# Optimization experiments

Measured on AMD Instinct MI355X. Metric: run time of the kernel, lower is better.

Reference implementation:

```python
import jax, jax.numpy as jnp
import numpy as np

B, N = 16384, 4096
PERCENT_ON = 0.1
TEMPERATURE = 10.0  # training-mode temperature
K = int(round(N * PERCENT_ON))  # 410


def setup_inputs() -> dict:
    key = jax.random.key(0)
    k1, k2 = jax.random.split(key)
    x = jax.random.normal(k1, (B, N), dtype=jnp.float32)
    # Gumbel noise for sampling-without-replacement (Gumbel-top-k trick),
    # equivalent to torch.multinomial(softmax(x/T), k, replacement=False).
    gumbel = jax.random.gumbel(k2, (B, N), dtype=jnp.float32)
    return {"x": x, "gumbel": gumbel}


def reference(x, gumbel):
    # logits with temperature
    logits = x / TEMPERATURE
    # entropy of the categorical distribution per row, averaged (single stable pass)
    logp = jax.nn.log_softmax(logits, axis=-1)
    entropy = jnp.mean(-jnp.sum(jnp.exp(logp) * logp, axis=-1))
    # sample K winners without replacement via Gumbel-top-k
    _, idx = jax.lax.top_k(logits + gumbel, K)  # idx: [B, K]
    rows = jnp.arange(x.shape[0])[:, None]       # [B, 1]
    mask = jnp.zeros_like(x).at[rows, idx].set(1.0)
    out = x * mask  # relu=False path
    return out, entropy
```

## Files before the change

### kernel.cpp

```cpp
#include <hip/hip_runtime.h>
#include <math.h>

#define TPB 256
#define EPT 16
#define NN  4096
#define KSEL 410
#define CAP 1024

typedef float floatx4 __attribute__((ext_vector_type(4)));

template <bool USE_WS>
__global__ __launch_bounds__(TPB, 8)
void skw_main(const float* __restrict__ x, const float* __restrict__ g,
              float* __restrict__ out, float* __restrict__ rowH,
              float* __restrict__ entAcc, float invB)
{
    const int row  = blockIdx.x;
    const int t    = threadIdx.x;
    const int w    = t >> 6;
    const int lane = t & 63;
    const size_t rbase = (size_t)row * NN;

    float    xv[EPT];
    unsigned bp[EPT / 4];

    __shared__ float    s_lds[NN];
    __shared__ unsigned hist0[256][5];
    __shared__ unsigned wtot[4];
    __shared__ unsigned wtA[4], wtB[4];
    __shared__ float    fred[8];
    __shared__ unsigned sh_digit, sh_above, sh_cnt, sh_take, sh_eq;
    __shared__ float    sh_thr;

    float*   list = reinterpret_cast<float*>(&hist0[0][0]);
    floatx4* s4   = reinterpret_cast<floatx4*>(s_lds);

    const float4* xp = reinterpret_cast<const float4*>(x + rbase);
    const float4* gp = reinterpret_cast<const float4*>(g + rbase);
    floatx4*      op = reinterpret_cast<floatx4*>(out + rbase);

    float sZ = 0.f, sZL = 0.f;
#pragma unroll
    for (int q = 0; q < EPT / 4; ++q) {
        float4 xx = xp[(q << 8) + t];
        float4 gg = gp[(q << 8) + t];
        float xa[4] = {xx.x, xx.y, xx.z, xx.w};
        float ga[4] = {gg.x, gg.y, gg.z, gg.w};
        floatx4 so;
        unsigned pk = 0;
#pragma unroll
        for (int jj = 0; jj < 4; ++jj) {
            float xs = xa[jj];
            xv[4 * q + jj] = xs;
            float l = xs * 0.1f;
            float e = __expf(l);
            sZ  += e;
            sZL = __builtin_fmaf(e, l, sZL);
            float q10 = __builtin_fmaf(__builtin_fmaf(-10.0f, l, xs), 0.1f, l);
            float s = q10 + ga[jj];
            so[jj] = s;
            int b = (int)__builtin_fmaf(s, 16.0f, 64.0f);
            b = min(max(b, 0), 255);
            pk |= (unsigned)b << (8 * jj);
        }
        s4[(q << 8) + t] = so;
        bp[q] = pk;
    }

#pragma unroll
    for (int sft = 32; sft >= 1; sft >>= 1) { sZ += __shfl_xor(sZ, sft); sZL += __shfl_xor(sZL, sft); }
    if (lane == 0) { fred[w] = sZ; fred[4 + w] = sZL; }

    unsigned* h0 = &hist0[0][0];
#pragma unroll
    for (int i = 0; i < 5; ++i) h0[t + 256 * i] = 0;
    if (t == 0) sh_cnt = 0;
    __syncthreads();

    if (t == 0) {
        float Z = fred[0] + fred[1] + fred[2] + fred[3];
        float L = fred[4] + fred[5] + fred[6] + fred[7];
        float H = __logf(Z) - L / Z;
        if (USE_WS) rowH[row] = H;
        else atomicAdd(entAcc, H * invB);
    }

#pragma unroll
    for (int q = 0; q < EPT / 4; ++q) {
        unsigned pk = bp[q];
#pragma unroll
        for (int jj = 0; jj < 4; ++jj)
            atomicAdd(&hist0[(pk >> (8 * jj)) & 255u][lane & 3], 1u);
    }
    __syncthreads();

    unsigned v = hist0[t][0] + hist0[t][1] + hist0[t][2] + hist0[t][3];
#pragma unroll
    for (int sft = 1; sft < 64; sft <<= 1) {
        unsigned tmp = __shfl(v, lane + sft);
        v += (lane + sft < 64) ? tmp : 0u;
    }
    if (lane == 0) wtot[w] = v;
    unsigned vnext = __shfl(v, lane + 1);
    __syncthreads();
    unsigned Kr = KSEL;
    {
        unsigned hi = 0;
#pragma unroll
        for (int c = 0; c < 4; ++c) hi += (c > w) ? wtot[c] : 0u;
        unsigned cum     = v + hi;
        unsigned cumNext = ((lane < 63) ? vnext : 0u) + hi;
        if (cum >= Kr && cumNext < Kr) { sh_digit = (unsigned)t; sh_above = cumNext; }
    }
    __syncthreads();
    const unsigned Bstar = sh_digit;
    Kr -= sh_above;

#pragma unroll
    for (int q = 0; q < EPT / 4; ++q) {
        unsigned pk = bp[q];
#pragma unroll
        for (int jj = 0; jj < 4; ++jj) {
            if (((pk >> (8 * jj)) & 255u) == Bstar) {
                unsigned p = atomicAdd(&sh_cnt, 1u);
                if (p < CAP) list[p] = s_lds[(q << 10) + 4 * t + jj];
            }
        }
    }
    __syncthreads();

    const unsigned M = sh_cnt;
    for (unsigned i = t; i < M; i += TPB) {
        float ki = list[i];
        unsigned gt = 0, eqc = 0;
        for (unsigned j2 = 0; j2 < M; ++j2) {
            float kj = list[j2];
            gt  += (kj > ki)  ? 1u : 0u;
            eqc += (kj == ki) ? 1u : 0u;
        }
        if (gt < Kr && Kr <= gt + eqc) { sh_thr = ki; sh_take = Kr - gt; sh_eq = eqc; }
    }
    __syncthreads();
    const float    thr    = sh_thr;
    const unsigned KrTake = sh_take;
    const unsigned EqTot  = sh_eq;

    if (KrTake == EqTot) {
#pragma unroll
        for (int q = 0; q < EPT / 4; ++q) {
            floatx4 sq = s4[(q << 8) + t];
            floatx4 o4;
#pragma unroll
            for (int jj = 0; jj < 4; ++jj)
                o4[jj] = (sq[jj] >= thr) ? xv[4 * q + jj] : 0.0f;
            __builtin_nontemporal_store(o4, &op[(q << 8) + t]);
        }
    } else {
        unsigned eq[4];
#pragma unroll
        for (int q = 0; q < 4; ++q) {
            floatx4 sq = s4[(q << 8) + t];
            unsigned e = 0;
#pragma unroll
            for (int jj = 0; jj < 4; ++jj) e += (sq[jj] == thr) ? 1u : 0u;
            eq[q] = e;
        }
        unsigned wA = eq[0] | (eq[1] << 16);
        unsigned wB = eq[2] | (eq[3] << 16);
        unsigned sA = wA, sB = wB;
#pragma unroll
        for (int sft = 1; sft < 64; sft <<= 1) {
            unsigned ta = __shfl(sA, lane - sft);
            unsigned tb = __shfl(sB, lane - sft);
            if (lane >= sft) { sA += ta; sB += tb; }
        }
        if (lane == 63) { wtA[w] = sA; wtB[w] = sB; }
        __syncthreads();
        unsigned offA = 0, offB = 0, totA = 0, totB = 0;
#pragma unroll
        for (int c = 0; c < 4; ++c) {
            totA += wtA[c]; totB += wtB[c];
            if (c < w) { offA += wtA[c]; offB += wtB[c]; }
        }
        unsigned exA = offA + sA - wA;
        unsigned exB = offB + sB - wB;
        unsigned tot0 = totA & 0xFFFFu, tot1 = totA >> 16, tot2 = totB & 0xFFFFu;
        unsigned baseq[4] = {0u, tot0, tot0 + tot1, tot0 + tot1 + tot2};
        unsigned exq[4]   = {exA & 0xFFFFu, exA >> 16, exB & 0xFFFFu, exB >> 16};

#pragma unroll
        for (int q = 0; q < EPT / 4; ++q) {
            unsigned pos = baseq[q] + exq[q];
            floatx4 sq = s4[(q << 8) + t];
            floatx4 o4;
#pragma unroll
            for (int jj = 0; jj < 4; ++jj) {
                bool sel;
                if (sq[jj] > thr)        sel = true;
                else if (sq[jj] == thr)  { sel = (pos < KrTake); ++pos; }
                else                     sel = false;
                o4[jj] = sel ? xv[4 * q + jj] : 0.0f;
            }
            __builtin_nontemporal_store(o4, &op[(q << 8) + t]);
        }
    }
}

__global__ void skw_zero(float* p) { *p = 0.0f; }

__global__ void skw_reduce(const float* __restrict__ rowH, float* __restrict__ outp, int B)
{
    __shared__ float red[256];
    int t = threadIdx.x;
    float s = 0.f;
    for (int i = t; i < B; i += 256) s += rowH[i];
    red[t] = s; __syncthreads();
    for (int st = 128; st > 0; st >>= 1) { if (t < st) red[t] += red[t + st]; __syncthreads(); }
    if (t == 0) *outp = red[0] / (float)B;
}

extern "C" void kernel_launch(void* const* d_in, const int* in_sizes, int n_in,
                              void* d_out, int out_size, void* d_ws, size_t ws_size,
                              hipStream_t stream)
{
    const float* x = (const float*)d_in[0];
    const float* g = (const float*)d_in[1];
    float* out = (float*)d_out;
    const int BN = in_sizes[0];
    const int B  = BN / NN;
    float* entp = out + (size_t)BN;

    if (ws_size >= (size_t)B * sizeof(float)) {
        float* rowH = (float*)d_ws;
        skw_main<true><<<B, TPB, 0, stream>>>(x, g, out, rowH, nullptr, 0.f);
        skw_reduce<<<1, 256, 0, stream>>>(rowH, entp, B);
    } else {
        skw_zero<<<1, 1, 0, stream>>>(entp);
        skw_main<false><<<B, TPB, 0, stream>>>(x, g, out, nullptr, entp, 1.0f / (float)B);
    }
}
```

Measured before the change: 165.3 us.

## Stage x and gumbel rows into LDS via direct global-to-LDS loads

```diff
diff --git a/kernel.cpp b/kernel.cpp
--- a/kernel.cpp
+++ b/kernel.cpp
@@ -9,8 +9,15 @@
 
 typedef float floatx4 __attribute__((ext_vector_type(4)));
 
+__device__ __forceinline__ void dma16(const float* gsrc, float* lds) {
+    __builtin_amdgcn_global_load_lds(
+        (__attribute__((address_space(1))) void*)(void*)gsrc,
+        (__attribute__((address_space(3))) void*)(void*)lds,
+        16, 0, 0);
+}
+
 template <bool USE_WS>
-__global__ __launch_bounds__(TPB, 8)
+__global__ __launch_bounds__(TPB)
 void skw_main(const float* __restrict__ x, const float* __restrict__ g,
               float* __restrict__ out, float* __restrict__ rowH,
               float* __restrict__ entAcc, float invB)
@@ -21,10 +28,9 @@
     const int lane = t & 63;
     const size_t rbase = (size_t)row * NN;
 
-    float    xv[EPT];
     unsigned bp[EPT / 4];
 
-    __shared__ float    s_lds[NN];
+    __shared__ float    stage[2 * NN];
     __shared__ unsigned hist0[256][5];
     __shared__ unsigned wtot[4];
     __shared__ unsigned wtA[4], wtB[4];
@@ -33,48 +39,55 @@
     __shared__ float    sh_thr;
 
     float*   list = reinterpret_cast<float*>(&hist0[0][0]);
-    floatx4* s4   = reinterpret_cast<floatx4*>(s_lds);
-
-    const float4* xp = reinterpret_cast<const float4*>(x + rbase);
-    const float4* gp = reinterpret_cast<const float4*>(g + rbase);
-    floatx4*      op = reinterpret_cast<floatx4*>(out + rbase);
+    floatx4* sx4  = reinterpret_cast<floatx4*>(stage);
+    floatx4* ss4  = reinterpret_cast<floatx4*>(stage + NN);
+
+    const float* xr = x + rbase;
+    const float* gr = g + rbase;
+    floatx4*     op = reinterpret_cast<floatx4*>(out + rbase);
+
+#pragma unroll
+    for (int q = 0; q < 4; ++q) {
+        const int c = (q << 2) + w;
+        dma16(xr + (c << 8) + (lane << 2), &stage[c << 8]);
+        dma16(gr + (c << 8) + (lane << 2), &stage[NN + (c << 8)]);
+    }
+
+    unsigned* h0 = &hist0[0][0];
+#pragma unroll
+    for (int i = 0; i < 5; ++i) h0[t + 256 * i] = 0;
+    if (t == 0) sh_cnt = 0;
+
+    asm volatile("s_waitcnt vmcnt(0)" ::: "memory");
 
     float sZ = 0.f, sZL = 0.f;
 #pragma unroll
     for (int q = 0; q < EPT / 4; ++q) {
-        float4 xx = xp[(q << 8) + t];
-        float4 gg = gp[(q << 8) + t];
-        float xa[4] = {xx.x, xx.y, xx.z, xx.w};
-        float ga[4] = {gg.x, gg.y, gg.z, gg.w};
+        floatx4 xx = sx4[(q << 8) + t];
+        floatx4 gg = ss4[(q << 8) + t];
         floatx4 so;
         unsigned pk = 0;
 #pragma unroll
         for (int jj = 0; jj < 4; ++jj) {
-            float xs = xa[jj];
-            xv[4 * q + jj] = xs;
+            float xs = xx[jj];
             float l = xs * 0.1f;
             float e = __expf(l);
             sZ  += e;
             sZL = __builtin_fmaf(e, l, sZL);
             float q10 = __builtin_fmaf(__builtin_fmaf(-10.0f, l, xs), 0.1f, l);
-            float s = q10 + ga[jj];
+            float s = q10 + gg[jj];
             so[jj] = s;
             int b = (int)__builtin_fmaf(s, 16.0f, 64.0f);
             b = min(max(b, 0), 255);
             pk |= (unsigned)b << (8 * jj);
         }
-        s4[(q << 8) + t] = so;
+        ss4[(q << 8) + t] = so;
         bp[q] = pk;
     }
 
 #pragma unroll
     for (int sft = 32; sft >= 1; sft >>= 1) { sZ += __shfl_xor(sZ, sft); sZL += __shfl_xor(sZL, sft); }
     if (lane == 0) { fred[w] = sZ; fred[4 + w] = sZL; }
-
-    unsigned* h0 = &hist0[0][0];
-#pragma unroll
-    for (int i = 0; i < 5; ++i) h0[t + 256 * i] = 0;
-    if (t == 0) sh_cnt = 0;
     __syncthreads();
 
     if (t == 0) {
@@ -123,7 +136,7 @@
         for (int jj = 0; jj < 4; ++jj) {
             if (((pk >> (8 * jj)) & 255u) == Bstar) {
                 unsigned p = atomicAdd(&sh_cnt, 1u);
-                if (p < CAP) list[p] = s_lds[(q << 10) + 4 * t + jj];
+                if (p < CAP) list[p] = stage[NN + (q << 10) + 4 * t + jj];
             }
         }
     }
@@ -148,18 +161,19 @@
     if (KrTake == EqTot) {
 #pragma unroll
         for (int q = 0; q < EPT / 4; ++q) {
-            floatx4 sq = s4[(q << 8) + t];
+            floatx4 sq = ss4[(q << 8) + t];
+            floatx4 xq = sx4[(q << 8) + t];
             floatx4 o4;
 #pragma unroll
             for (int jj = 0; jj < 4; ++jj)
-                o4[jj] = (sq[jj] >= thr) ? xv[4 * q + jj] : 0.0f;
+                o4[jj] = (sq[jj] >= thr) ? xq[jj] : 0.0f;
             __builtin_nontemporal_store(o4, &op[(q << 8) + t]);
         }
     } else {
         unsigned eq[4];
 #pragma unroll
         for (int q = 0; q < 4; ++q) {
-            floatx4 sq = s4[(q << 8) + t];
+            floatx4 sq = ss4[(q << 8) + t];
             unsigned e = 0;
 #pragma unroll
             for (int jj = 0; jj < 4; ++jj) e += (sq[jj] == thr) ? 1u : 0u;
@@ -191,7 +205,8 @@
 #pragma unroll
         for (int q = 0; q < EPT / 4; ++q) {
             unsigned pos = baseq[q] + exq[q];
-            floatx4 sq = s4[(q << 8) + t];
+            floatx4 sq = ss4[(q << 8) + t];
+            floatx4 xq = sx4[(q << 8) + t];
             floatx4 o4;
 #pragma unroll
             for (int jj = 0; jj < 4; ++jj) {
@@ -199,7 +214,7 @@
                 if (sq[jj] > thr)        sel = true;
                 else if (sq[jj] == thr)  { sel = (pos < KrTake); ++pos; }
                 else                     sel = false;
-                o4[jj] = sel ? xv[4 * q + jj] : 0.0f;
+                o4[jj] = sel ? xq[jj] : 0.0f;
             }
             __builtin_nontemporal_store(o4, &op[(q << 8) + t]);
         }
```

Measured after the change: 163.3 us, median of 4. Within noise of the previous version (-1.2%).
